# Kernel tuning notes

Measured on AMD Instinct MI355X. Metric: run time of the kernel, lower is better.

The kernel has to match this reference:

```python
import jax, jax.numpy as jnp
import numpy as np

K = 3            # pairwise_size
DIL = 2          # pairwise_dilation
COLOR_THRESH = 0.3
EOS_COEF = 0.1


def unfold_wo_center(x, k, d):
    """x: [N,1,H,W] -> [N,1,k*k-1,H,W]; zero-padded dilated neighborhood, center removed
    (equivalent to F.unfold(x, k, padding=(k//2)*d, dilation=d) minus center tap)."""
    N, C, H, W = x.shape
    pad = (k // 2) * d
    xp = jnp.pad(x, ((0, 0), (0, 0), (pad, pad), (pad, pad)))
    c = k // 2
    patches = []
    for i in range(k):
        for j in range(k):
            if i == c and j == c:
                continue
            patches.append(xp[:, :, i * d:i * d + H, j * d:j * d + W])
    return jnp.stack(patches, axis=2)


def setup_inputs() -> dict:
    key = jax.random.key(0)
    k1, k2, k3, k4, k5 = jax.random.split(key, 5)
    B, Q, C1 = 2, 100, 81          # batch, queries, num_classes+1
    N, H, W = 64, 256, 256         # matched instances, mask resolution
    pred_logits = jax.random.normal(k1, (B, Q, C1), jnp.float32)
    target_classes = jax.random.randint(k2, (B, Q), 0, C1)
    src_masks = jax.random.normal(k3, (N, H, W), jnp.float32)
    target_box_masks = jax.random.randint(k4, (N, H, W), 0, 2).astype(jnp.int32)
    target_similarities = jax.random.uniform(k5, (N, K * K - 1, H, W), jnp.float32)
    empty_weight = jnp.ones((C1,), jnp.float32).at[-1].set(EOS_COEF)
    return {
        "pred_logits": pred_logits,
        "src_masks": src_masks,
        "empty_weight": empty_weight,
        "target_similarities": target_similarities,
        "target_classes": target_classes,
        "target_box_masks": target_box_masks,
        "num_masks": 64,
    }


def reference(pred_logits, src_masks, empty_weight, target_similarities,
              target_classes, target_box_masks, num_masks):
    nm = jnp.float32(max(int(num_masks), 1))

    # ---- loss_labels: weighted cross entropy (PyTorch weighted mean) ----
    logp = jax.nn.log_softmax(pred_logits.astype(jnp.float32), axis=-1)
    nll = -jnp.take_along_axis(logp, target_classes[..., None], axis=-1)[..., 0]
    w = empty_weight[target_classes]
    loss_ce = (w * nll).sum() / w.sum()

    # ---- loss_pairwise: BoxInst-style log-prob affinity over dilated neighborhood ----
    x = src_masks[:, None]                      # [N,1,H,W]
    lfg = jax.nn.log_sigmoid(x)
    lbg = jax.nn.log_sigmoid(-x)
    fg_u = unfold_wo_center(lfg, K, DIL)        # [N,1,8,H,W]
    bg_u = unfold_wo_center(lbg, K, DIL)
    a = lfg[:, :, None] + fg_u                  # log P(both fg)
    b = lbg[:, :, None] + bg_u                  # log P(both bg)
    m = jnp.maximum(a, b)
    log_same = jnp.log(jnp.exp(a - m) + jnp.exp(b - m)) + m
    sim = -log_same[:, 0]                       # [N,8,H,W]
    tgt = (target_similarities >= COLOR_THRESH).astype(jnp.float32) \
          * target_box_masks[:, None].astype(jnp.float32)
    loss_pairwise = (sim * tgt).sum() / jnp.maximum(tgt.sum(), 1.0) / nm
    # warmup_factor = 1.0 (iter >= pairwise_warmup_iters)

    # ---- loss_projection_masks: 1D projection dice ----
    eps = 0.001
    tb = target_box_masks.astype(jnp.float32)
    ix = jax.nn.sigmoid(src_masks.max(axis=2))  # project over W -> [N,H]
    iy = jax.nn.sigmoid(src_masks.max(axis=1))  # project over H -> [N,W]
    tx = tb.max(axis=2)
    ty = tb.max(axis=1)
    lx = 1.0 - 2.0 * (ix * tx).sum(1) / ((ix ** 2).sum(1) + (tx ** 2).sum(1) + eps)
    ly = 1.0 - 2.0 * (iy * ty).sum(1) / ((iy ** 2).sum(1) + (ty ** 2).sum(1) + eps)
    loss_proj = (lx + ly).sum() / nm

    return loss_ce + loss_pairwise + loss_proj
```

## Files before the change

### kernel.cpp

```cpp
#include <hip/hip_runtime.h>
#include <hip/hip_bf16.h>
#include <cmath>

#define H 256
#define W 256
#define NIMG 64
#define HW 65536
#define RG 8
#define NROWG 32

__device__ inline float waveReduceSum(float v) {
#pragma unroll
    for (int o = 32; o > 0; o >>= 1) v += __shfl_xor(v, o, 64);
    return v;
}
__device__ inline float waveReduceMax(float v) {
#pragma unroll
    for (int o = 32; o > 0; o >>= 1) v = fmaxf(v, __shfl_xor(v, o, 64));
    return v;
}
__device__ inline float blockReduceSum(float v, float* s) {
    int lane = threadIdx.x & 63, wv = threadIdx.x >> 6;
    v = waveReduceSum(v);
    if (lane == 0) s[wv] = v;
    __syncthreads();
    float r = 0.f;
    if (wv == 0) {
        r = (lane < 4) ? s[lane] : 0.f;
        r = waveReduceSum(r);
    }
    __syncthreads();
    return r;
}

__global__ __launch_bounds__(256) void k_pairwise(
    const float* __restrict__ src, const float* __restrict__ ts,
    const int* __restrict__ bm,
    float* __restrict__ part_st, float* __restrict__ part_t,
    float* __restrict__ rowsig, float* __restrict__ rowmax_b,
    float* __restrict__ colpart_s, float* __restrict__ colpart_b)
{
    __shared__ float s_sig[12][264];
    __shared__ float red[4];
    const int hg = blockIdx.x, n = blockIdx.y, t = threadIdx.x;
    const int h0 = hg * RG;
    const int lane = t & 63, wv = t >> 6;
    const float* srcn = src + (size_t)n * HW;

    if (t < 96) {
        const int row = t >> 3, j = t & 7;
        const int idx = (j < 4) ? j : (256 + j);
        s_sig[row][idx] = 0.5f;
    }
#pragma unroll
    for (int k = 0; k < 3; k++) {
        const int idx = t + k * 256;
        const int row = idx >> 6;
        const int col = (idx & 63) << 2;
        const int gr = h0 - 2 + row;
        float4 xv = make_float4(0.f, 0.f, 0.f, 0.f);
        if (gr >= 0 && gr < H) xv = *reinterpret_cast<const float4*>(srcn + gr * W + col);
        float4 sv;
        sv.x = __builtin_amdgcn_rcpf(1.f + __expf(-xv.x));
        sv.y = __builtin_amdgcn_rcpf(1.f + __expf(-xv.y));
        sv.z = __builtin_amdgcn_rcpf(1.f + __expf(-xv.z));
        sv.w = __builtin_amdgcn_rcpf(1.f + __expf(-xv.w));
        *reinterpret_cast<float4*>(&s_sig[row][4 + col]) = sv;
    }
    __syncthreads();

    const int* bmn = bm + (size_t)n * HW;
    const float* tsn = ts + (size_t)n * 8 * HW;
    const int c0 = lane << 2;

    float st = 0.f, tt = 0.f;
    float cms[4] = {0.f, 0.f, 0.f, 0.f};
    float cmb[4] = {0.f, 0.f, 0.f, 0.f};

#pragma unroll
    for (int rr = wv; rr < RG; rr += 4) {
        const int h = h0 + rr;
        const int ci = rr + 2;
        const bool rvt = (h - 2) >= 0;
        const bool rvb = (h + 2) < H;

        const int4 bi = *reinterpret_cast<const int4*>(bmn + h * W + c0);
        float4 tv[8];
#pragma unroll
        for (int p = 0; p < 8; p++)
            tv[p] = *reinterpret_cast<const float4*>(tsn + (size_t)p * HW + h * W + c0);

        float ftop[12], fmid[12], fbot[12];
        *reinterpret_cast<float4*>(&ftop[0]) = *reinterpret_cast<const float4*>(&s_sig[ci - 2][c0]);
        *reinterpret_cast<float4*>(&ftop[4]) = *reinterpret_cast<const float4*>(&s_sig[ci - 2][c0 + 4]);
        *reinterpret_cast<float4*>(&ftop[8]) = *reinterpret_cast<const float4*>(&s_sig[ci - 2][c0 + 8]);
        *reinterpret_cast<float4*>(&fmid[0]) = *reinterpret_cast<const float4*>(&s_sig[ci][c0]);
        *reinterpret_cast<float4*>(&fmid[4]) = *reinterpret_cast<const float4*>(&s_sig[ci][c0 + 4]);
        *reinterpret_cast<float4*>(&fmid[8]) = *reinterpret_cast<const float4*>(&s_sig[ci][c0 + 8]);
        *reinterpret_cast<float4*>(&fbot[0]) = *reinterpret_cast<const float4*>(&s_sig[ci + 2][c0]);
        *reinterpret_cast<float4*>(&fbot[4]) = *reinterpret_cast<const float4*>(&s_sig[ci + 2][c0 + 4]);
        *reinterpret_cast<float4*>(&fbot[8]) = *reinterpret_cast<const float4*>(&s_sig[ci + 2][c0 + 8]);

        const float* tvp = reinterpret_cast<const float*>(tv);
        float msc = 0.f, mb = 0.f;
#pragma unroll
        for (int p = 0; p < 4; p++) {
            const float sc = fmid[4 + p];
            const float a2 = 2.f * sc;
            const float b2 = 1.f - sc;
            const float bmf = (float)reinterpret_cast<const int*>(&bi)[p];
            const bool cl = (c0 + p - 2) >= 0;
            const bool cr = (c0 + p + 2) < W;
            msc = fmaxf(msc, sc); mb = fmaxf(mb, bmf);
            cms[p] = fmaxf(cms[p], sc); cmb[p] = fmaxf(cmb[p], bmf);

            float prod = 1.f, cnt = 0.f;
            auto tap = [&](float sn, bool valid, float tsv) {
                const bool thr = (tsv >= 0.3f);
                cnt += thr ? 1.f : 0.f;
                const float P = fmaf(a2, sn, b2 - sn);
                prod *= (thr && valid) ? P : 1.f;
            };
            tap(ftop[2 + p], rvt && cl, tvp[0 * 4 + p]);
            tap(ftop[4 + p], rvt,       tvp[1 * 4 + p]);
            tap(ftop[6 + p], rvt && cr, tvp[2 * 4 + p]);
            tap(fmid[2 + p], cl,        tvp[3 * 4 + p]);
            tap(fmid[6 + p], cr,        tvp[4 * 4 + p]);
            tap(fbot[2 + p], rvb && cl, tvp[5 * 4 + p]);
            tap(fbot[4 + p], rvb,       tvp[6 * 4 + p]);
            tap(fbot[6 + p], rvb && cr, tvp[7 * 4 + p]);

            st = fmaf(bmf, -__logf(prod), st);
            tt = fmaf(bmf, cnt, tt);
        }
        const float wms = waveReduceMax(msc);
        const float wmb = waveReduceMax(mb);
        if (lane == 0) {
            rowsig[n * H + h] = wms;
            rowmax_b[n * H + h] = wmb;
        }
    }
    const int co = (n * NROWG + hg) * W + c0;
    *reinterpret_cast<float4*>(&colpart_s[co]) = make_float4(cms[0], cms[1], cms[2], cms[3]);
    *reinterpret_cast<float4*>(&colpart_b[co]) = make_float4(cmb[0], cmb[1], cmb[2], cmb[3]);

    const float sst = blockReduceSum(st, red);
    const float stt = blockReduceSum(tt, red);
    if (t == 0) {
        const int o = n * NROWG + hg;
        part_st[o] = sst;
        part_t[o] = stt;
    }
}

__global__ __launch_bounds__(256) void k_proj(
    const float* __restrict__ colpart_s, const float* __restrict__ colpart_b,
    const float* __restrict__ rowsig, const float* __restrict__ rowmax_b,
    float* __restrict__ proj)
{
    __shared__ float red[4];
    const int n = blockIdx.x, t = threadIdx.x;
    float cs = 0.f, cb = 0.f;
#pragma unroll 8
    for (int c = 0; c < NROWG; c++) {
        cs = fmaxf(cs, colpart_s[(n * NROWG + c) * W + t]);
        cb = fmaxf(cb, colpart_b[(n * NROWG + c) * W + t]);
    }
    const float iy = cs;
    const float ty = cb;
    const float ix = rowsig[n * H + t];
    const float tx = rowmax_b[n * H + t];

    const float Sxy = blockReduceSum(ix * tx, red);
    const float Sxx = blockReduceSum(ix * ix, red);
    const float Stx = blockReduceSum(tx * tx, red);
    const float Syw = blockReduceSum(iy * ty, red);
    const float Syy = blockReduceSum(iy * iy, red);
    const float Sty = blockReduceSum(ty * ty, red);
    if (t == 0) {
        const float eps = 0.001f;
        const float lx = 1.f - 2.f * Sxy / (Sxx + Stx + eps);
        const float ly = 1.f - 2.f * Syw / (Syy + Sty + eps);
        proj[n] = lx + ly;
    }
}

__global__ __launch_bounds__(256) void k_final(
    const float* __restrict__ logits, const int* __restrict__ tcls,
    const float* __restrict__ ew, const int* __restrict__ num_masks,
    const float* __restrict__ part_st, const float* __restrict__ part_t,
    const float* __restrict__ proj, float* __restrict__ out)
{
    __shared__ float red[4];
    const int t = threadIdx.x;
    float s1 = 0.f, s2 = 0.f;
    for (int i = t; i < NIMG * NROWG; i += 256) { s1 += part_st[i]; s2 += part_t[i]; }
    const float sum_st = blockReduceSum(s1, red);
    const float sum_t = blockReduceSum(s2, red);
    const float pj = (t < NIMG) ? proj[t] : 0.f;
    const float sum_pj = blockReduceSum(pj, red);

    float wn = 0.f, wsum = 0.f;
    if (t < 200) {
        const float* row = logits + t * 81;
        float mx = -3.4e38f;
        for (int c = 0; c < 81; c++) mx = fmaxf(mx, row[c]);
        float se = 0.f;
        for (int c = 0; c < 81; c++) se += expf(row[c] - mx);
        const float lse = mx + logf(se);
        const int tc = tcls[t];
        const float nll = lse - row[tc];
        const float wv = ew[tc];
        wn = wv * nll;
        wsum = wv;
    }
    const float Swn = blockReduceSum(wn, red);
    const float Sw = blockReduceSum(wsum, red);
    if (t == 0) {
        const float nm = (float)max(num_masks[0], 1);
        const float loss_ce = Swn / Sw;
        const float loss_pw = sum_st / fmaxf(sum_t, 1.f) / nm;
        const float loss_pj = sum_pj / nm;
        out[0] = loss_ce + loss_pw + loss_pj;
    }
}

extern "C" void kernel_launch(void* const* d_in, const int* in_sizes, int n_in,
                              void* d_out, int out_size, void* d_ws, size_t ws_size,
                              hipStream_t stream) {
    const float* pred_logits = (const float*)d_in[0];
    const float* src         = (const float*)d_in[1];
    const float* ew          = (const float*)d_in[2];
    const float* ts          = (const float*)d_in[3];
    const int*   tcls        = (const int*)d_in[4];
    const int*   bm          = (const int*)d_in[5];
    const int*   nmasks      = (const int*)d_in[6];
    float* out = (float*)d_out;

    float* ws = (float*)d_ws;
    float* part_st   = ws;
    float* part_t    = ws + 2048;
    float* rowsig    = ws + 4096;
    float* rowmax_b  = ws + 20480;
    float* colpart_s = ws + 36864;
    float* colpart_b = ws + 561152;
    float* proj      = ws + 1085440;

    k_pairwise<<<dim3(NROWG, NIMG), 256, 0, stream>>>(src, ts, bm, part_st, part_t,
                                                      rowsig, rowmax_b, colpart_s, colpart_b);
    k_proj<<<NIMG, 256, 0, stream>>>(colpart_s, colpart_b, rowsig, rowmax_b, proj);
    k_final<<<1, 256, 0, stream>>>(pred_logits, tcls, ew, nmasks, part_st, part_t, proj, out);
}
```

Before: 260.3 us.

## Replace shared-memory sigmoid tile with per-wave register strips using shuffles

Each wave now handles a strip of 4 rows with the same row parity (stride 2), keeping three sigmoid rows in registers as a rolling window. Horizontal neighbours come from wave shuffles instead of shared memory, and the next source row is prefetched during the current row. This removes the LDS tile, its barrier and the block-level reductions in the main kernel. The cost is twice as many column partials (64 strips per image) for the projection kernel to reduce, and a little less sigmoid reuse per strip.

```diff
diff --git a/kernel.cpp b/kernel.cpp
--- a/kernel.cpp
+++ b/kernel.cpp
@@ -6,8 +6,8 @@
 #define W 256
 #define NIMG 64
 #define HW 65536
-#define RG 8
-#define NROWG 32
+#define NSTRIP 64
+#define TOTSTRIP (NIMG * NSTRIP)
 
 __device__ inline float waveReduceSum(float v) {
 #pragma unroll
@@ -33,6 +33,15 @@
     return r;
 }
 
+__device__ inline float4 sig4(float4 x) {
+    float4 s;
+    s.x = __builtin_amdgcn_rcpf(1.f + __expf(-x.x));
+    s.y = __builtin_amdgcn_rcpf(1.f + __expf(-x.y));
+    s.z = __builtin_amdgcn_rcpf(1.f + __expf(-x.z));
+    s.w = __builtin_amdgcn_rcpf(1.f + __expf(-x.w));
+    return s;
+}
+
 __global__ __launch_bounds__(256) void k_pairwise(
     const float* __restrict__ src, const float* __restrict__ ts,
     const int* __restrict__ bm,
@@ -40,47 +49,44 @@
     float* __restrict__ rowsig, float* __restrict__ rowmax_b,
     float* __restrict__ colpart_s, float* __restrict__ colpart_b)
 {
-    __shared__ float s_sig[12][264];
-    __shared__ float red[4];
-    const int hg = blockIdx.x, n = blockIdx.y, t = threadIdx.x;
-    const int h0 = hg * RG;
-    const int lane = t & 63, wv = t >> 6;
+    const int t = threadIdx.x, lane = t & 63, wv = t >> 6;
+    const int strip = blockIdx.x * 4 + wv;
+    const int n = strip >> 6, sid = strip & 63;
+    const int parity = sid & 1, g = sid >> 1;
+    const int h0 = g * 8 + parity;
+    const int c0 = lane << 2;
+    const int lm = (lane + 63) & 63, lp = (lane + 1) & 63;
+
     const float* srcn = src + (size_t)n * HW;
-
-    if (t < 96) {
-        const int row = t >> 3, j = t & 7;
-        const int idx = (j < 4) ? j : (256 + j);
-        s_sig[row][idx] = 0.5f;
-    }
-#pragma unroll
-    for (int k = 0; k < 3; k++) {
-        const int idx = t + k * 256;
-        const int row = idx >> 6;
-        const int col = (idx & 63) << 2;
-        const int gr = h0 - 2 + row;
-        float4 xv = make_float4(0.f, 0.f, 0.f, 0.f);
-        if (gr >= 0 && gr < H) xv = *reinterpret_cast<const float4*>(srcn + gr * W + col);
-        float4 sv;
-        sv.x = __builtin_amdgcn_rcpf(1.f + __expf(-xv.x));
-        sv.y = __builtin_amdgcn_rcpf(1.f + __expf(-xv.y));
-        sv.z = __builtin_amdgcn_rcpf(1.f + __expf(-xv.z));
-        sv.w = __builtin_amdgcn_rcpf(1.f + __expf(-xv.w));
-        *reinterpret_cast<float4*>(&s_sig[row][4 + col]) = sv;
-    }
-    __syncthreads();
-
-    const int* bmn = bm + (size_t)n * HW;
-    const float* tsn = ts + (size_t)n * 8 * HW;
-    const int c0 = lane << 2;
+    const int*   bmn  = bm  + (size_t)n * HW;
+    const float* tsn  = ts  + (size_t)n * 8 * HW;
+
+    auto loadRaw = [&](int r) -> float4 {
+        float4 x = make_float4(0.f, 0.f, 0.f, 0.f);
+        if (r >= 0 && r < H) x = *reinterpret_cast<const float4*>(srcn + r * W + c0);
+        return x;
+    };
+    auto finishRow = [&](float4 x, float* o) {
+        float4 s = sig4(x);
+        o[2] = s.x; o[3] = s.y; o[4] = s.z; o[5] = s.w;
+        o[0] = __shfl(s.z, lm, 64);
+        o[1] = __shfl(s.w, lm, 64);
+        o[6] = __shfl(s.x, lp, 64);
+        o[7] = __shfl(s.y, lp, 64);
+    };
+
+    float A[8], B[8], C[8];
+    finishRow(loadRaw(h0 - 2), A);
+    finishRow(loadRaw(h0),     B);
+    finishRow(loadRaw(h0 + 2), C);
 
     float st = 0.f, tt = 0.f;
     float cms[4] = {0.f, 0.f, 0.f, 0.f};
     float cmb[4] = {0.f, 0.f, 0.f, 0.f};
 
 #pragma unroll
-    for (int rr = wv; rr < RG; rr += 4) {
-        const int h = h0 + rr;
-        const int ci = rr + 2;
+    for (int j = 0; j < 4; j++) {
+        const int h = h0 + 2 * j;
         const bool rvt = (h - 2) >= 0;
         const bool rvb = (h + 2) < H;
 
@@ -89,23 +95,14 @@
 #pragma unroll
         for (int p = 0; p < 8; p++)
             tv[p] = *reinterpret_cast<const float4*>(tsn + (size_t)p * HW + h * W + c0);
-
-        float ftop[12], fmid[12], fbot[12];
-        *reinterpret_cast<float4*>(&ftop[0]) = *reinterpret_cast<const float4*>(&s_sig[ci - 2][c0]);
-        *reinterpret_cast<float4*>(&ftop[4]) = *reinterpret_cast<const float4*>(&s_sig[ci - 2][c0 + 4]);
-        *reinterpret_cast<float4*>(&ftop[8]) = *reinterpret_cast<const float4*>(&s_sig[ci - 2][c0 + 8]);
-        *reinterpret_cast<float4*>(&fmid[0]) = *reinterpret_cast<const float4*>(&s_sig[ci][c0]);
-        *reinterpret_cast<float4*>(&fmid[4]) = *reinterpret_cast<const float4*>(&s_sig[ci][c0 + 4]);
-        *reinterpret_cast<float4*>(&fmid[8]) = *reinterpret_cast<const float4*>(&s_sig[ci][c0 + 8]);
-        *reinterpret_cast<float4*>(&fbot[0]) = *reinterpret_cast<const float4*>(&s_sig[ci + 2][c0]);
-        *reinterpret_cast<float4*>(&fbot[4]) = *reinterpret_cast<const float4*>(&s_sig[ci + 2][c0 + 4]);
-        *reinterpret_cast<float4*>(&fbot[8]) = *reinterpret_cast<const float4*>(&s_sig[ci + 2][c0 + 8]);
+        float4 nxtraw = make_float4(0.f, 0.f, 0.f, 0.f);
+        if (j < 3) nxtraw = loadRaw(h + 4);
 
         const float* tvp = reinterpret_cast<const float*>(tv);
         float msc = 0.f, mb = 0.f;
 #pragma unroll
         for (int p = 0; p < 4; p++) {
-            const float sc = fmid[4 + p];
+            const float sc = B[2 + p];
             const float a2 = 2.f * sc;
             const float b2 = 1.f - sc;
             const float bmf = (float)reinterpret_cast<const int*>(&bi)[p];
@@ -121,14 +118,14 @@
                 const float P = fmaf(a2, sn, b2 - sn);
                 prod *= (thr && valid) ? P : 1.f;
             };
-            tap(ftop[2 + p], rvt && cl, tvp[0 * 4 + p]);
-            tap(ftop[4 + p], rvt,       tvp[1 * 4 + p]);
-            tap(ftop[6 + p], rvt && cr, tvp[2 * 4 + p]);
-            tap(fmid[2 + p], cl,        tvp[3 * 4 + p]);
-            tap(fmid[6 + p], cr,        tvp[4 * 4 + p]);
-            tap(fbot[2 + p], rvb && cl, tvp[5 * 4 + p]);
-            tap(fbot[4 + p], rvb,       tvp[6 * 4 + p]);
-            tap(fbot[6 + p], rvb && cr, tvp[7 * 4 + p]);
+            tap(A[p],     rvt && cl, tvp[0 * 4 + p]);
+            tap(A[2 + p], rvt,       tvp[1 * 4 + p]);
+            tap(A[4 + p], rvt && cr, tvp[2 * 4 + p]);
+            tap(B[p],     cl,        tvp[3 * 4 + p]);
+            tap(B[4 + p], cr,        tvp[4 * 4 + p]);
+            tap(C[p],     rvb && cl, tvp[5 * 4 + p]);
+            tap(C[2 + p], rvb,       tvp[6 * 4 + p]);
+            tap(C[4 + p], rvb && cr, tvp[7 * 4 + p]);
 
             st = fmaf(bmf, -__logf(prod), st);
             tt = fmaf(bmf, cnt, tt);
@@ -139,17 +136,22 @@
             rowsig[n * H + h] = wms;
             rowmax_b[n * H + h] = wmb;
         }
-    }
-    const int co = (n * NROWG + hg) * W + c0;
+        if (j < 3) {
+#pragma unroll
+            for (int i = 0; i < 8; i++) { A[i] = B[i]; B[i] = C[i]; }
+            finishRow(nxtraw, C);
+        }
+    }
+
+    const int co = (n * NSTRIP + sid) * W + c0;
     *reinterpret_cast<float4*>(&colpart_s[co]) = make_float4(cms[0], cms[1], cms[2], cms[3]);
     *reinterpret_cast<float4*>(&colpart_b[co]) = make_float4(cmb[0], cmb[1], cmb[2], cmb[3]);
 
-    const float sst = blockReduceSum(st, red);
-    const float stt = blockReduceSum(tt, red);
-    if (t == 0) {
-        const int o = n * NROWG + hg;
-        part_st[o] = sst;
-        part_t[o] = stt;
+    const float wst = waveReduceSum(st);
+    const float wtt = waveReduceSum(tt);
+    if (lane == 0) {
+        part_st[strip] = wst;
+        part_t[strip] = wtt;
     }
 }
 
@@ -162,9 +164,9 @@
     const int n = blockIdx.x, t = threadIdx.x;
     float cs = 0.f, cb = 0.f;
 #pragma unroll 8
-    for (int c = 0; c < NROWG; c++) {
-        cs = fmaxf(cs, colpart_s[(n * NROWG + c) * W + t]);
-        cb = fmaxf(cb, colpart_b[(n * NROWG + c) * W + t]);
+    for (int c = 0; c < NSTRIP; c++) {
+        cs = fmaxf(cs, colpart_s[(n * NSTRIP + c) * W + t]);
+        cb = fmaxf(cb, colpart_b[(n * NSTRIP + c) * W + t]);
     }
     const float iy = cs;
     const float ty = cb;
@@ -194,7 +196,7 @@
     __shared__ float red[4];
     const int t = threadIdx.x;
     float s1 = 0.f, s2 = 0.f;
-    for (int i = t; i < NIMG * NROWG; i += 256) { s1 += part_st[i]; s2 += part_t[i]; }
+    for (int i = t; i < TOTSTRIP; i += 256) { s1 += part_st[i]; s2 += part_t[i]; }
     const float sum_st = blockReduceSum(s1, red);
     const float sum_t = blockReduceSum(s2, red);
     const float pj = (t < NIMG) ? proj[t] : 0.f;
@@ -239,15 +241,15 @@
 
     float* ws = (float*)d_ws;
     float* part_st   = ws;
-    float* part_t    = ws + 2048;
-    float* rowsig    = ws + 4096;
-    float* rowmax_b  = ws + 20480;
-    float* colpart_s = ws + 36864;
-    float* colpart_b = ws + 561152;
-    float* proj      = ws + 1085440;
-
-    k_pairwise<<<dim3(NROWG, NIMG), 256, 0, stream>>>(src, ts, bm, part_st, part_t,
-                                                      rowsig, rowmax_b, colpart_s, colpart_b);
+    float* part_t    = ws + 4096;
+    float* rowsig    = ws + 8192;
+    float* rowmax_b  = ws + 24576;
+    float* colpart_s = ws + 40960;
+    float* colpart_b = ws + 1089536;
+    float* proj      = ws + 2138112;
+
+    k_pairwise<<<dim3(TOTSTRIP / 4), 256, 0, stream>>>(src, ts, bm, part_st, part_t,
+                                                       rowsig, rowmax_b, colpart_s, colpart_b);
     k_proj<<<NIMG, 256, 0, stream>>>(colpart_s, colpart_b, rowsig, rowmax_b, proj);
     k_final<<<1, 256, 0, stream>>>(pred_logits, tcls, ew, nmasks, part_st, part_t, proj, out);
 }
```

After: 263.5 us. No clear change (+1.2%).
